# Optimization experiments

Hardware: AMD Instinct MI355X
Metric: run time of the kernel (lower is better)

The kernel has to match this reference:

```python
import jax, jax.numpy as jnp
import numpy as np

B, N, M, D = 4, 4096, 4096, 128


def setup_inputs() -> dict:
    key = jax.random.key(0)
    kk, kq, kv = jax.random.split(key, 3)
    return {
        "k": jax.random.normal(kk, (B, N, D), dtype=jnp.float32),
        "q": jax.random.normal(kq, (B, M, D), dtype=jnp.float32),
        "v": jax.random.normal(kv, (B, M, D), dtype=jnp.float32),
    }


def reference(k, q, v):
    # scores: [B, N, M] = k @ q^T
    scores = jnp.einsum("bnd,bmd->bnm", k, q)
    # Original uses nn.Softmax() with no dim; torch's legacy rule resolves
    # dim=0 for 3-D inputs, so softmax is over the batch axis, applied twice.
    w = jax.nn.softmax(jax.nn.softmax(scores, axis=0), axis=0)
    out = jnp.einsum("bnm,bmd->bnd", w, v)
    return out
```

## Files before the change

kernel.cpp:

```cpp
#include <hip/hip_runtime.h>
#include <hip/hip_bf16.h>

#define NB 4
#define NN 4096
#define MM 4096
#define DD 128
#define BN 32
#define BM 64
#define NCH 4
#define OUT_ELEMS ((size_t)NB * NN * DD)

using f32x4  = __attribute__((ext_vector_type(4))) float;
using bf16x8 = __attribute__((ext_vector_type(8))) short;

__device__ __forceinline__ float fast_exp2(float x) {
  return __builtin_amdgcn_exp2f(x);
}

__device__ __forceinline__ int rfl(int x) {
  return __builtin_amdgcn_readfirstlane(x);
}

__device__ __forceinline__ short f2bf(float x) {
  union { __hip_bfloat16 h; short s; } u;
  u.h = __float2bfloat16(x);
  return u.s;
}

__device__ __forceinline__ float bf2f(unsigned short s) {
  union { float f; unsigned u; } u;
  u.u = ((unsigned)s) << 16;
  return u.f;
}

__device__ __forceinline__ bf16x8 pack8(const float* __restrict__ p) {
  float4 a = *(const float4*)p;
  float4 b = *(const float4*)(p + 4);
  bf16x8 r;
  r[0] = f2bf(a.x); r[1] = f2bf(a.y); r[2] = f2bf(a.z); r[3] = f2bf(a.w);
  r[4] = f2bf(b.x); r[5] = f2bf(b.y); r[6] = f2bf(b.z); r[7] = f2bf(b.w);
  return r;
}

__global__ __launch_bounds__(256) void zero_out_kernel(float4* __restrict__ out) {
  out[(size_t)blockIdx.x * 256 + threadIdx.x] = (float4){0.f, 0.f, 0.f, 0.f};
}

__global__ __launch_bounds__(256) void cvt_frag_kernel(const float* __restrict__ s0,
                                                       const float* __restrict__ s1,
                                                       unsigned short* __restrict__ d0,
                                                       unsigned short* __restrict__ d1) {
  const float* src = blockIdx.y ? s1 : s0;
  unsigned short* dst = blockIdx.y ? d1 : d0;
  const int blk = blockIdx.x;
  const int b = blk >> 8, rf = blk & 255;
  const int kf = threadIdx.x >> 6, l = threadIdx.x & 63;
  const int lr = l & 15, hg = l >> 4;
  const float* s = src + ((size_t)(b * 4096 + rf * 16 + lr) * DD + kf * 32 + hg * 8);
  bf16x8 r = pack8(s);
  *(bf16x8*)(dst + (((size_t)((b * 256 + rf) * 4 + kf)) << 9) + (l << 3)) = r;
}

__global__ __launch_bounds__(256) void transpose_v_frag_kernel(const float* __restrict__ v,
                                                               unsigned short* __restrict__ vt) {
  __shared__ unsigned short t[64][72];
  const int b = blockIdx.z, d0 = blockIdx.y * 64, m0 = blockIdx.x * 64;
  const int r = threadIdx.x >> 2, c4 = threadIdx.x & 3;
  const float* src = v + ((size_t)b * MM + m0 + r) * DD + d0 + c4 * 16;
  for (int j = 0; j < 4; ++j) {
    float4 x = *(const float4*)(src + j * 4);
    int dl = c4 * 16 + j * 4;
    t[dl + 0][r] = (unsigned short)f2bf(x.x);
    t[dl + 1][r] = (unsigned short)f2bf(x.y);
    t[dl + 2][r] = (unsigned short)f2bf(x.z);
    t[dl + 3][r] = (unsigned short)f2bf(x.w);
  }
  __syncthreads();
  const int s8 = threadIdx.x >> 5;
  const int dfl = s8 & 3, mtl = s8 >> 2;
  const int t32 = threadIdx.x & 31;
  for (int ll = 0; ll < 2; ++ll) {
    const int l = t32 * 2 + ll;
    const int lr = l & 15, hg = l >> 4;
    bf16x8 val = *(bf16x8*)&t[dfl * 16 + lr][mtl * 32 + hg * 8];
    *(bf16x8*)(vt + (((size_t)((b * 8 + (d0 >> 4) + dfl) * 128 + (m0 >> 5) + mtl)) << 9) +
               (l << 3)) = val;
  }
}

__global__ __launch_bounds__(256) void reduce4_frag_kernel(const float* __restrict__ p,
                                                           float* __restrict__ out) {
  const size_t idx = (size_t)blockIdx.x * 256 + threadIdx.x;
  f32x4 r = *(const f32x4*)(p + idx * 4);
  for (int c = 1; c < NCH; ++c) {
    f32x4 a = *(const f32x4*)(p + (size_t)c * OUT_ELEMS + idx * 4);
    r[0] += a[0]; r[1] += a[1]; r[2] += a[2]; r[3] += a[3];
  }
  const int l = (int)(idx & 63);
  const int djg = (int)((idx >> 6) & 7);
  const int nf = (int)((idx >> 9) & 255);
  const int bq = (int)(idx >> 17);
  const int lr = l & 15, hg = l >> 4;
  float* o = out + ((size_t)(bq * 4096 + nf * 16 + hg * 4) * DD + djg * 16 + lr);
  o[0] = r[0]; o[DD] = r[1]; o[2 * DD] = r[2]; o[3 * DD] = r[3];
}

#define LGKM0_SBAR()                                        \
  do {                                                      \
    asm volatile("s_waitcnt lgkmcnt(0)" ::: "memory");      \
    __builtin_amdgcn_sched_barrier(0);                      \
    __builtin_amdgcn_s_barrier();                           \
  } while (0)

template <bool WS, bool PART>
__global__ __launch_bounds__(512, 4) void attn_fused(
    const float* __restrict__ k, const float* __restrict__ q, const float* __restrict__ v,
    const unsigned short* __restrict__ kbt, const unsigned short* __restrict__ qbt,
    const unsigned short* __restrict__ vtt, float* __restrict__ outp) {
  __shared__ alignas(8)  unsigned short s_pos[NB][8][64][4];
  __shared__ alignas(16) unsigned short Wl[NB][BN][BM];

  const int tid = threadIdx.x;
  const int wv = tid >> 6, l = tid & 63, lr = l & 15, hg = l >> 4;
  const int voff = l << 3;
  const int wg = blockIdx.x;
  const int cid = wg & (NCH - 1);
  const int n0 = (wg >> 2) * BN;
  const int it0 = cid * (MM / BM / NCH);
  const int it1 = it0 + (MM / BM / NCH);

  const int bq = wv >> 1, h = wv & 1;
  const int h_s = wv >> 2, fi_s = (wv >> 1) & 1, fj_s = wv & 1;

  bf16x8 ka[2][4];
  {
    const unsigned short* kp = WS ? (kbt + rfl(((bq * 256 + (n0 >> 4)) * 4) << 9)) : nullptr;
    for (int fn = 0; fn < 2; ++fn)
      for (int kf = 0; kf < 4; ++kf) {
        if (WS) ka[fn][kf] = *(const bf16x8*)(kp + fn * 2048 + kf * 512 + voff);
        else    ka[fn][kf] = pack8(k + ((size_t)bq * NN + n0 + fn * 16 + lr) * DD +
                                   kf * 32 + hg * 8);
      }
  }

  f32x4 acc[2][4];
  for (int fi = 0; fi < 2; ++fi)
    for (int dj = 0; dj < 4; ++dj) acc[fi][dj] = (f32x4){0.f, 0.f, 0.f, 0.f};

  bf16x8 vf[4][2];
  bf16x8 qf[2][4];

  auto load_q = [&](int it) {
    if (WS) {
      const unsigned short* qp = qbt + rfl(((bq * 256 + it * 4 + h * 2) * 4) << 9);
      for (int fm = 0; fm < 2; ++fm)
        for (int kf = 0; kf < 4; ++kf)
          qf[fm][kf] = *(const bf16x8*)(qp + fm * 2048 + kf * 512 + voff);
    } else {
      const int m0 = it * BM;
      for (int fm = 0; fm < 2; ++fm)
        for (int kf = 0; kf < 4; ++kf)
          qf[fm][kf] = pack8(q + ((size_t)bq * MM + m0 + h * 32 + fm * 16 + lr) * DD +
                             kf * 32 + hg * 8);
    }
  };

  auto qk_mfma = [&]() {
    f32x4 s[2][2];
    for (int fm = 0; fm < 2; ++fm)
      for (int fn = 0; fn < 2; ++fn) s[fm][fn] = (f32x4){0.f, 0.f, 0.f, 0.f};
    __builtin_amdgcn_s_setprio(1);
    for (int kf = 0; kf < 4; ++kf)
      for (int fm = 0; fm < 2; ++fm)
        for (int fn = 0; fn < 2; ++fn)
          s[fm][fn] = __builtin_amdgcn_mfma_f32_16x16x32_bf16(qf[fm][kf], ka[fn][kf],
                                                              s[fm][fn], 0, 0, 0);
    __builtin_amdgcn_s_setprio(0);
    for (int fm = 0; fm < 2; ++fm)
      for (int fn = 0; fn < 2; ++fn) {
        short4 pk;
        pk.x = f2bf(s[fm][fn][0]); pk.y = f2bf(s[fm][fn][1]);
        pk.z = f2bf(s[fm][fn][2]); pk.w = f2bf(s[fm][fn][3]);
        *(short4*)&s_pos[bq][h * 4 + fm * 2 + fn][l][0] = pk;
      }
  };

  auto issue_v = [&](int it) {
    if (WS) {
      const unsigned short* vp = vtt + rfl((((bq * 8 + h * 4) * 128) + it * 2) << 9);
      for (int dj = 0; dj < 4; ++dj)
        for (int kf = 0; kf < 2; ++kf)
          vf[dj][kf] = *(const bf16x8*)(vp + dj * 65536 + kf * 512 + voff);
    } else {
      const int m0 = it * BM;
      for (int dj = 0; dj < 4; ++dj)
        for (int kf = 0; kf < 2; ++kf) {
          bf16x8 t;
          for (int e = 0; e < 8; ++e)
            t[e] = f2bf(v[((size_t)bq * MM + m0 + kf * 32 + hg * 8 + e) * DD +
                          h * 64 + dj * 16 + lr]);
          vf[dj][kf] = t;
        }
    }
  };

  auto do_sm = [&]() {
    float sv[NB][4], w[NB][4];
    for (int bb = 0; bb < NB; ++bb) {
      short4 sp = *(short4*)&s_pos[bb][wv][l][0];
      sv[bb][0] = bf2f((unsigned short)sp.x); sv[bb][1] = bf2f((unsigned short)sp.y);
      sv[bb][2] = bf2f((unsigned short)sp.z); sv[bb][3] = bf2f((unsigned short)sp.w);
    }
    const float L2E = 1.4426950408889634f;
    for (int qq = 0; qq < 4; ++qq) {
      float e0 = fast_exp2(sv[0][qq] * L2E), e1 = fast_exp2(sv[1][qq] * L2E);
      float e2 = fast_exp2(sv[2][qq] * L2E), e3 = fast_exp2(sv[3][qq] * L2E);
      float inv = __builtin_amdgcn_rcpf((e0 + e1) + (e2 + e3)) * L2E;
      float f0 = fast_exp2(e0 * inv), f1 = fast_exp2(e1 * inv);
      float f2v = fast_exp2(e2 * inv), f3 = fast_exp2(e3 * inv);
      float inv2 = __builtin_amdgcn_rcpf((f0 + f1) + (f2v + f3));
      w[0][qq] = f0 * inv2; w[1][qq] = f1 * inv2;
      w[2][qq] = f2v * inv2; w[3][qq] = f3 * inv2;
    }
    const int n_loc = fj_s * 16 + lr;
    const int mchunk = (h_s * 4 + fi_s * 2 + (hg >> 1)) ^ (n_loc & 7);
    const int moff = mchunk * 8 + (hg & 1) * 4;
    for (int bb = 0; bb < NB; ++bb) {
      short4 pk;
      pk.x = f2bf(w[bb][0]); pk.y = f2bf(w[bb][1]);
      pk.z = f2bf(w[bb][2]); pk.w = f2bf(w[bb][3]);
      *(short4*)&Wl[bb][n_loc][moff] = pk;
    }
  };

  auto do_pv = [&]() {
    bf16x8 wf[2][2];
    for (int fi = 0; fi < 2; ++fi)
      for (int kf = 0; kf < 2; ++kf) {
        const int row = fi * 16 + lr, mo = kf * 32 + hg * 8;
        wf[fi][kf] = *(bf16x8*)&Wl[bq][row][mo ^ ((row & 7) << 3)];
      }
    __builtin_amdgcn_s_setprio(1);
    for (int kf = 0; kf < 2; ++kf)
      for (int fi = 0; fi < 2; ++fi)
        for (int dj = 0; dj < 4; ++dj)
          acc[fi][dj] = __builtin_amdgcn_mfma_f32_16x16x32_bf16(wf[fi][kf], vf[dj][kf],
                                                                acc[fi][dj], 0, 0, 0);
    __builtin_amdgcn_s_setprio(0);
  };

  load_q(it0);
  qk_mfma();
  LGKM0_SBAR();
  for (int t = it0; t < it1; ++t) {
    issue_v(t);
    do_sm();
    LGKM0_SBAR();
    do_pv();
    if (t + 1 < it1) {
      load_q(t + 1);
      qk_mfma();
    }
    LGKM0_SBAR();
  }

  if (PART) {
    float* dst = outp + (size_t)cid * OUT_ELEMS +
                 rfl((((bq * 256 + (n0 >> 4)) * 8 + h * 4)) << 8);
    for (int fi = 0; fi < 2; ++fi)
      for (int dj = 0; dj < 4; ++dj)
        *(f32x4*)(dst + fi * 2048 + dj * 256 + (l << 2)) = acc[fi][dj];
  } else {
    float* dst = outp;
    for (int fi = 0; fi < 2; ++fi)
      for (int dj = 0; dj < 4; ++dj)
        for (int qq = 0; qq < 4; ++qq)
          atomicAdd(dst + ((size_t)bq * NN + n0 + fi * 16 + hg * 4 + qq) * DD +
                        h * 64 + dj * 16 + lr,
                    acc[fi][dj][qq]);
  }
}

extern "C" void kernel_launch(void* const* d_in, const int* in_sizes, int n_in,
                              void* d_out, int out_size, void* d_ws, size_t ws_size,
                              hipStream_t stream) {
  (void)in_sizes; (void)n_in; (void)out_size;
  const float* k = (const float*)d_in[0];
  const float* q = (const float*)d_in[1];
  const float* v = (const float*)d_in[2];
  float* out = (float*)d_out;

  const size_t elems = (size_t)NB * MM * DD;
  const size_t need_bf = 3 * elems * sizeof(unsigned short);
  const size_t need_full = need_bf + NCH * OUT_ELEMS * sizeof(float);
  const bool use_ws = (d_ws != nullptr) && (ws_size >= need_bf);
  const bool use_part = (d_ws != nullptr) && (ws_size >= need_full);

  if (use_ws) {
    unsigned short* kbt = (unsigned short*)d_ws;
    unsigned short* qbt = kbt + elems;
    unsigned short* vtt = qbt + elems;
    cvt_frag_kernel<<<dim3(NB * 256, 2), 256, 0, stream>>>(k, q, kbt, qbt);
    transpose_v_frag_kernel<<<dim3(MM / 64, DD / 64, NB), 256, 0, stream>>>(v, vtt);
    if (use_part) {
      float* partials = (float*)((char*)d_ws + need_bf);
      attn_fused<true, true><<<dim3(NN / BN * NCH), 512, 0, stream>>>(k, q, v, kbt, qbt, vtt,
                                                                      partials);
      reduce4_frag_kernel<<<2048, 256, 0, stream>>>(partials, out);
    } else {
      zero_out_kernel<<<(NB * NN * DD) / 4 / 256, 256, 0, stream>>>((float4*)out);
      attn_fused<true, false><<<dim3(NN / BN * NCH), 512, 0, stream>>>(k, q, v, kbt, qbt, vtt,
                                                                       out);
    }
  } else {
    zero_out_kernel<<<(NB * NN * DD) / 4 / 256, 256, 0, stream>>>((float4*)out);
    attn_fused<false, false><<<dim3(NN / BN * NCH), 512, 0, stream>>>(k, q, v, nullptr,
                                                                      nullptr, nullptr, out);
  }
}
```

Baseline: 79.27 us.

## Double-buffer score and weight LDS tiles to skew PV one step behind

Adds a second LDS buffer for both the QK score tile and the softmax weight tile. The loop is restructured so the PV MFMA for the previous tile runs at the start of each iteration, followed by the V and Q loads, the softmax and the next QK. This cuts the number of block-wide barriers per iteration from two to one and lets memory loads overlap with matrix work. The cost is doubled LDS use per workgroup, which may lower the number of resident workgroups per CU below the launch-bounds target.

Measured after the change: 125.4 us. +58.2%, slower.

```diff
diff --git a/kernel.cpp b/kernel.cpp
--- a/kernel.cpp
+++ b/kernel.cpp
@@ -117,8 +117,8 @@
     const float* __restrict__ k, const float* __restrict__ q, const float* __restrict__ v,
     const unsigned short* __restrict__ kbt, const unsigned short* __restrict__ qbt,
     const unsigned short* __restrict__ vtt, float* __restrict__ outp) {
-  __shared__ alignas(8)  unsigned short s_pos[NB][8][64][4];
-  __shared__ alignas(16) unsigned short Wl[NB][BN][BM];
+  __shared__ alignas(8)  unsigned short s_pos[2][NB][8][64][4];
+  __shared__ alignas(16) unsigned short Wl[2][NB][BN][BM];
 
   const int tid = threadIdx.x;
   const int wv = tid >> 6, l = tid & 63, lr = l & 15, hg = l >> 4;
@@ -165,7 +165,7 @@
     }
   };
 
-  auto qk_mfma = [&]() {
+  auto qk_mfma = [&](int buf) {
     f32x4 s[2][2];
     for (int fm = 0; fm < 2; ++fm)
       for (int fn = 0; fn < 2; ++fn) s[fm][fn] = (f32x4){0.f, 0.f, 0.f, 0.f};
@@ -181,7 +181,7 @@
         short4 pk;
         pk.x = f2bf(s[fm][fn][0]); pk.y = f2bf(s[fm][fn][1]);
         pk.z = f2bf(s[fm][fn][2]); pk.w = f2bf(s[fm][fn][3]);
-        *(short4*)&s_pos[bq][h * 4 + fm * 2 + fn][l][0] = pk;
+        *(short4*)&s_pos[buf][bq][h * 4 + fm * 2 + fn][l][0] = pk;
       }
   };
 
@@ -204,10 +204,10 @@
     }
   };
 
-  auto do_sm = [&]() {
+  auto do_sm = [&](int buf) {
     float sv[NB][4], w[NB][4];
     for (int bb = 0; bb < NB; ++bb) {
-      short4 sp = *(short4*)&s_pos[bb][wv][l][0];
+      short4 sp = *(short4*)&s_pos[buf][bb][wv][l][0];
       sv[bb][0] = bf2f((unsigned short)sp.x); sv[bb][1] = bf2f((unsigned short)sp.y);
       sv[bb][2] = bf2f((unsigned short)sp.z); sv[bb][3] = bf2f((unsigned short)sp.w);
     }
@@ -229,16 +229,16 @@
       short4 pk;
       pk.x = f2bf(w[bb][0]); pk.y = f2bf(w[bb][1]);
       pk.z = f2bf(w[bb][2]); pk.w = f2bf(w[bb][3]);
-      *(short4*)&Wl[bb][n_loc][moff] = pk;
-    }
-  };
-
-  auto do_pv = [&]() {
+      *(short4*)&Wl[buf][bb][n_loc][moff] = pk;
+    }
+  };
+
+  auto do_pv = [&](int buf) {
     bf16x8 wf[2][2];
     for (int fi = 0; fi < 2; ++fi)
       for (int kf = 0; kf < 2; ++kf) {
         const int row = fi * 16 + lr, mo = kf * 32 + hg * 8;
-        wf[fi][kf] = *(bf16x8*)&Wl[bq][row][mo ^ ((row & 7) << 3)];
+        wf[fi][kf] = *(bf16x8*)&Wl[buf][bq][row][mo ^ ((row & 7) << 3)];
       }
     __builtin_amdgcn_s_setprio(1);
     for (int kf = 0; kf < 2; ++kf)
@@ -250,19 +250,17 @@
   };
 
   load_q(it0);
-  qk_mfma();
+  qk_mfma(it0 & 1);
   LGKM0_SBAR();
   for (int t = it0; t < it1; ++t) {
+    if (t > it0) do_pv((t - 1) & 1);
     issue_v(t);
-    do_sm();
+    if (t + 1 < it1) load_q(t + 1);
+    do_sm(t & 1);
+    if (t + 1 < it1) qk_mfma((t + 1) & 1);
     LGKM0_SBAR();
-    do_pv();
-    if (t + 1 < it1) {
-      load_q(t + 1);
-      qk_mfma();
-    }
-    LGKM0_SBAR();
-  }
+  }
+  do_pv((it1 - 1) & 1);
 
   if (PART) {
     float* dst = outp + (size_t)cid * OUT_ELEMS +
```

## Double-buffer softmax weights to overlap PV with softmax; store partials in bf16

Applied to the files above, without the earlier changes.

Makes the LDS weight buffer double-buffered so the PV MFMA for the previous tile runs before the softmax of the current tile. This restructures the loop to cut one barrier-separated phase per iteration. Separately, the per-chunk partial outputs are written as bf16 instead of fp32, halving partial write and reduce read traffic. The cost is lower precision in the partial sums before the final reduction and more LDS use per block.

After: 103.9 us. +31.1%, slower.

```diff
diff --git a/kernel.cpp b/kernel.cpp
--- a/kernel.cpp
+++ b/kernel.cpp
@@ -88,13 +88,13 @@
   }
 }
 
-__global__ __launch_bounds__(256) void reduce4_frag_kernel(const float* __restrict__ p,
+__global__ __launch_bounds__(256) void reduce4_frag_kernel(const unsigned short* __restrict__ p,
                                                            float* __restrict__ out) {
   const size_t idx = (size_t)blockIdx.x * 256 + threadIdx.x;
-  f32x4 r = *(const f32x4*)(p + idx * 4);
-  for (int c = 1; c < NCH; ++c) {
-    f32x4 a = *(const f32x4*)(p + (size_t)c * OUT_ELEMS + idx * 4);
-    r[0] += a[0]; r[1] += a[1]; r[2] += a[2]; r[3] += a[3];
+  float r0 = 0.f, r1 = 0.f, r2 = 0.f, r3 = 0.f;
+  for (int c = 0; c < NCH; ++c) {
+    ushort4 a = *(const ushort4*)(p + (size_t)c * OUT_ELEMS + idx * 4);
+    r0 += bf2f(a.x); r1 += bf2f(a.y); r2 += bf2f(a.z); r3 += bf2f(a.w);
   }
   const int l = (int)(idx & 63);
   const int djg = (int)((idx >> 6) & 7);
@@ -102,7 +102,7 @@
   const int bq = (int)(idx >> 17);
   const int lr = l & 15, hg = l >> 4;
   float* o = out + ((size_t)(bq * 4096 + nf * 16 + hg * 4) * DD + djg * 16 + lr);
-  o[0] = r[0]; o[DD] = r[1]; o[2 * DD] = r[2]; o[3 * DD] = r[3];
+  o[0] = r0; o[DD] = r1; o[2 * DD] = r2; o[3 * DD] = r3;
 }
 
 #define LGKM0_SBAR()                                        \
@@ -116,9 +116,9 @@
 __global__ __launch_bounds__(512, 4) void attn_fused(
     const float* __restrict__ k, const float* __restrict__ q, const float* __restrict__ v,
     const unsigned short* __restrict__ kbt, const unsigned short* __restrict__ qbt,
-    const unsigned short* __restrict__ vtt, float* __restrict__ outp) {
+    const unsigned short* __restrict__ vtt, void* __restrict__ outp) {
   __shared__ alignas(8)  unsigned short s_pos[NB][8][64][4];
-  __shared__ alignas(16) unsigned short Wl[NB][BN][BM];
+  __shared__ alignas(16) unsigned short Wl[2][NB][BN][BM];
 
   const int tid = threadIdx.x;
   const int wv = tid >> 6, l = tid & 63, lr = l & 15, hg = l >> 4;
@@ -204,7 +204,7 @@
     }
   };
 
-  auto do_sm = [&]() {
+  auto do_sm = [&](int buf) {
     float sv[NB][4], w[NB][4];
     for (int bb = 0; bb < NB; ++bb) {
       short4 sp = *(short4*)&s_pos[bb][wv][l][0];
@@ -229,16 +229,16 @@
       short4 pk;
       pk.x = f2bf(w[bb][0]); pk.y = f2bf(w[bb][1]);
       pk.z = f2bf(w[bb][2]); pk.w = f2bf(w[bb][3]);
-      *(short4*)&Wl[bb][n_loc][moff] = pk;
-    }
-  };
-
-  auto do_pv = [&]() {
+      *(short4*)&Wl[buf][bb][n_loc][moff] = pk;
+    }
+  };
+
+  auto do_pv = [&](int buf) {
     bf16x8 wf[2][2];
     for (int fi = 0; fi < 2; ++fi)
       for (int kf = 0; kf < 2; ++kf) {
         const int row = fi * 16 + lr, mo = kf * 32 + hg * 8;
-        wf[fi][kf] = *(bf16x8*)&Wl[bq][row][mo ^ ((row & 7) << 3)];
+        wf[fi][kf] = *(bf16x8*)&Wl[buf][bq][row][mo ^ ((row & 7) << 3)];
       }
     __builtin_amdgcn_s_setprio(1);
     for (int kf = 0; kf < 2; ++kf)
@@ -253,25 +253,31 @@
   qk_mfma();
   LGKM0_SBAR();
   for (int t = it0; t < it1; ++t) {
+    if (t > it0) do_pv((t - 1) & 1);
+    do_sm(t & 1);
+    __builtin_amdgcn_sched_barrier(0);
     issue_v(t);
-    do_sm();
     LGKM0_SBAR();
-    do_pv();
     if (t + 1 < it1) {
       load_q(t + 1);
       qk_mfma();
     }
     LGKM0_SBAR();
   }
+  do_pv((it1 - 1) & 1);
 
   if (PART) {
-    float* dst = outp + (size_t)cid * OUT_ELEMS +
-                 rfl((((bq * 256 + (n0 >> 4)) * 8 + h * 4)) << 8);
+    unsigned short* dst = (unsigned short*)outp + (size_t)cid * OUT_ELEMS +
+                          rfl((((bq * 256 + (n0 >> 4)) * 8 + h * 4)) << 8);
     for (int fi = 0; fi < 2; ++fi)
-      for (int dj = 0; dj < 4; ++dj)
-        *(f32x4*)(dst + fi * 2048 + dj * 256 + (l << 2)) = acc[fi][dj];
+      for (int dj = 0; dj < 4; ++dj) {
+        short4 pk;
+        pk.x = f2bf(acc[fi][dj][0]); pk.y = f2bf(acc[fi][dj][1]);
+        pk.z = f2bf(acc[fi][dj][2]); pk.w = f2bf(acc[fi][dj][3]);
+        *(short4*)(dst + fi * 2048 + dj * 256 + (l << 2)) = pk;
+      }
   } else {
-    float* dst = outp;
+    float* dst = (float*)outp;
     for (int fi = 0; fi < 2; ++fi)
       for (int dj = 0; dj < 4; ++dj)
         for (int qq = 0; qq < 4; ++qq)
@@ -292,7 +298,7 @@
 
   const size_t elems = (size_t)NB * MM * DD;
   const size_t need_bf = 3 * elems * sizeof(unsigned short);
-  const size_t need_full = need_bf + NCH * OUT_ELEMS * sizeof(float);
+  const size_t need_full = need_bf + NCH * OUT_ELEMS * sizeof(unsigned short);
   const bool use_ws = (d_ws != nullptr) && (ws_size >= need_bf);
   const bool use_part = (d_ws != nullptr) && (ws_size >= need_full);
 
@@ -303,18 +309,19 @@
     cvt_frag_kernel<<<dim3(NB * 256, 2), 256, 0, stream>>>(k, q, kbt, qbt);
     transpose_v_frag_kernel<<<dim3(MM / 64, DD / 64, NB), 256, 0, stream>>>(v, vtt);
     if (use_part) {
-      float* partials = (float*)((char*)d_ws + need_bf);
+      unsigned short* partials = vtt + elems;
       attn_fused<true, true><<<dim3(NN / BN * NCH), 512, 0, stream>>>(k, q, v, kbt, qbt, vtt,
-                                                                      partials);
+                                                                      (void*)partials);
       reduce4_frag_kernel<<<2048, 256, 0, stream>>>(partials, out);
     } else {
       zero_out_kernel<<<(NB * NN * DD) / 4 / 256, 256, 0, stream>>>((float4*)out);
       attn_fused<true, false><<<dim3(NN / BN * NCH), 512, 0, stream>>>(k, q, v, kbt, qbt, vtt,
-                                                                       out);
+                                                                       (void*)out);
     }
   } else {
     zero_out_kernel<<<(NB * NN * DD) / 4 / 256, 256, 0, stream>>>((float4*)out);
     attn_fused<false, false><<<dim3(NN / BN * NCH), 512, 0, stream>>>(k, q, v, nullptr,
-                                                                      nullptr, nullptr, out);
-  }
-}
+                                                                      nullptr, nullptr,
+                                                                      (void*)out);
+  }
+}
```
